# Kernel optimization log

Measured on AMD Instinct MI355X. Metric: run time of the kernel, lower is better.

Reference implementation:

```python
import jax, jax.numpy as jnp
import numpy as np

B, S, H = 4, 1024, 4096
NH, NKV, HD = 32, 8, 128
LEVEL = 256


def lsq_quant(x, s, sym):
    # LSQ fake quantization with grad-scale on s and STE round.
    if sym:
        qn, qp = -LEVEL // 2, LEVEL // 2 - 1
    else:
        qn, qp = 0, LEVEL - 1
    g = 1.0 / np.sqrt(x.size * qp)
    s_sc = s * g + jax.lax.stop_gradient(s - s * g)  # value == s, grad scaled by g
    xs = jnp.clip(x / s_sc, qn, qp)
    xq = xs + jax.lax.stop_gradient(jnp.round(xs) - xs)  # STE round
    return xq * s_sc


def rotate_half(x):
    d = x.shape[-1] // 2
    return jnp.concatenate([-x[..., d:], x[..., :d]], axis=-1)


def setup_inputs() -> dict:
    key = jax.random.key(0)
    ks = jax.random.split(key, 8)
    hidden_states = jax.random.normal(ks[0], (B, S, H), dtype=jnp.float32)
    # real RoPE tables (theta=10000)
    inv_freq = 1.0 / (10000.0 ** (np.arange(0, HD, 2, dtype=np.float32) / HD))
    pos = np.arange(S, dtype=np.float32)
    freqs = np.outer(pos, inv_freq)                      # [S, HD/2]
    emb = np.concatenate([freqs, freqs], axis=-1)        # [S, HD]
    cos = jnp.broadcast_to(jnp.cos(emb)[None], (B, S, HD)).astype(jnp.float32)
    sin = jnp.broadcast_to(jnp.sin(emb)[None], (B, S, HD)).astype(jnp.float32)
    # additive causal mask [B,1,S,S]
    neg = jnp.finfo(jnp.float32).min
    causal = jnp.where(jnp.tril(jnp.ones((S, S), bool)), 0.0, neg)
    attention_mask = jnp.broadcast_to(causal[None, None], (B, 1, S, S)).astype(jnp.float32)
    std = 1.0 / np.sqrt(H)
    Wq = jax.random.normal(ks[1], (NH * HD, H), dtype=jnp.float32) * std
    Wk = jax.random.normal(ks[2], (NKV * HD, H), dtype=jnp.float32) * std
    Wv = jax.random.normal(ks[3], (NKV * HD, H), dtype=jnp.float32) * std
    Wo = jax.random.normal(ks[4], (H, NH * HD), dtype=jnp.float32) * std
    return {
        "hidden_states": hidden_states, "cos": cos, "sin": sin,
        "attention_mask": attention_mask,
        "Wq": Wq, "Wk": Wk, "Wv": Wv, "Wo": Wo,
        "s_q": jnp.float32(0.05), "s_k": jnp.float32(0.05), "s_v": jnp.float32(0.05),
        "s_attn": jnp.float32(0.05), "s_after": jnp.float32(0.05), "s_o": jnp.float32(0.05),
    }


def reference(hidden_states, cos, sin, attention_mask, Wq, Wk, Wv, Wo,
              s_q, s_k, s_v, s_attn, s_after, s_o):
    b, s, _ = hidden_states.shape
    scaling = HD ** -0.5
    n_rep = NH // NKV
    # projections (torch Linear: x @ W^T), reshape to [B, heads, S, HD]
    q = (hidden_states @ Wq.T).reshape(b, s, NH, HD).transpose(0, 2, 1, 3)
    k = (hidden_states @ Wk.T).reshape(b, s, NKV, HD).transpose(0, 2, 1, 3)
    v = (hidden_states @ Wv.T).reshape(b, s, NKV, HD).transpose(0, 2, 1, 3)
    q = lsq_quant(q, s_q, sym=True)
    k = lsq_quant(k, s_k, sym=True)
    v = lsq_quant(v, s_v, sym=True)
    # rotary embeddings (cos/sin: [B,S,HD] -> broadcast over head dim)
    c = cos[:, None, :, :]
    sn = sin[:, None, :, :]
    q = q * c + rotate_half(q) * sn
    k = k * c + rotate_half(k) * sn
    # repeat KV heads for GQA
    k = jnp.repeat(k, n_rep, axis=1)
    v = jnp.repeat(v, n_rep, axis=1)
    attn = jnp.einsum('bhqd,bhkd->bhqk', q, k) * scaling
    attn = lsq_quant(attn, s_attn, sym=False)
    attn = attn + attention_mask
    attn = jax.nn.softmax(attn.astype(jnp.float32), axis=-1)
    out = jnp.einsum('bhqk,bhkd->bhqd', attn, v)
    out = lsq_quant(out, s_after, sym=False)
    out = out.transpose(0, 2, 1, 3).reshape(b, s, NH * HD)
    out = out @ Wo.T
    out = lsq_quant(out, s_o, sym=True)
    return out, attn
```

## Files before the change

kernel.cpp:

```cpp
#include <hip/hip_runtime.h>
#include <math.h>

#define B_   4
#define S_   1024
#define H_   4096
#define NH_  32
#define NKV_ 8
#define HD_  128
#define M_   (B_*S_)
#define LDF16 12288
#define SCALING 0.08838834764831845f


typedef _Float16 f16;
typedef __attribute__((ext_vector_type(4))) _Float16 f16x4;
typedef __attribute__((ext_vector_type(8))) _Float16 f16x8;
typedef __attribute__((ext_vector_type(4))) float f32x4;

__device__ __forceinline__ float lsq_sym(float x, float s) {
  float xs = x / s;
  xs = fminf(fmaxf(xs, -128.0f), 127.0f);
  return rintf(xs) * s;
}
__device__ __forceinline__ float lsq_asym(float x, float s) {
  float xs = x / s;
  xs = fminf(fmaxf(xs, 0.0f), 255.0f);
  return rintf(xs) * s;
}

struct f16pair { f16 hi, lo; };
__device__ __forceinline__ f16pair cvt_hilo(float x) {
  f16pair r;
  r.hi = (f16)x;
  r.lo = (f16)(x - (float)r.hi);
  return r;
}

__device__ __forceinline__ void gload16(const void* g, void* l) {
  __builtin_amdgcn_global_load_lds((const __attribute__((address_space(1))) void*)g,
                                   (__attribute__((address_space(3))) void*)l, 16, 0, 0);
}

__global__ __launch_bounds__(256)
void split_flat(const float* __restrict__ src, f16* __restrict__ hi, f16* __restrict__ lo)
{
  const size_t i = ((size_t)blockIdx.x * 256 + threadIdx.x) * 4;
  float4 v = *(const float4*)(src + i);
  f16x4 h, l; f16pair p;
  p = cvt_hilo(v.x); h.x = p.hi; l.x = p.lo;
  p = cvt_hilo(v.y); h.y = p.hi; l.y = p.lo;
  p = cvt_hilo(v.z); h.z = p.hi; l.z = p.lo;
  p = cvt_hilo(v.w); h.w = p.hi; l.w = p.lo;
  *(f16x4*)(hi + i) = h;
  *(f16x4*)(lo + i) = l;
}

__global__ __launch_bounds__(256)
void split_wqk(const float* __restrict__ W, f16* __restrict__ hi, f16* __restrict__ lo, int ldw)
{
  const size_t i = ((size_t)blockIdx.x * 256 + threadIdx.x) * 4;
  const int n = (int)(i / ldw);
  const int k = (int)(i % ldw);
  const int d = n & 127;
  const int prow = (n & ~127) | ((d < 64) ? (d << 1) : (((d - 64) << 1) | 1));
  float4 v = *(const float4*)(W + i);
  f16x4 h, l; f16pair p;
  p = cvt_hilo(v.x); h.x = p.hi; l.x = p.lo;
  p = cvt_hilo(v.y); h.y = p.hi; l.y = p.lo;
  p = cvt_hilo(v.z); h.z = p.hi; l.z = p.lo;
  p = cvt_hilo(v.w); h.w = p.hi; l.w = p.lo;
  *(f16x4*)(hi + (size_t)prow * ldw + k) = h;
  *(f16x4*)(lo + (size_t)prow * ldw + k) = l;
}

__global__ __launch_bounds__(256)
void split_wo(const float* __restrict__ Wo, f16* __restrict__ base)
{
  const size_t i = ((size_t)blockIdx.x * 256 + threadIdx.x) * 4;
  const int n = (int)(i >> 12);
  const int k = (int)(i & 4095);
  float4 v = *(const float4*)(Wo + i);
  f16x4 h, l; f16pair p;
  p = cvt_hilo(v.x); h.x = p.hi; l.x = p.lo;
  p = cvt_hilo(v.y); h.y = p.hi; l.y = p.lo;
  p = cvt_hilo(v.z); h.z = p.hi; l.z = p.lo;
  p = cvt_hilo(v.w); h.w = p.hi; l.w = p.lo;
  f16* rp = base + (size_t)n * LDF16;
  *(f16x4*)(rp + 4096 + k) = h;
  *(f16x4*)(rp + 8192 + k) = l;
}

template<int ATERMS, int EPI>
__global__ __launch_bounds__(256, 2)
void gemm_mfma(const f16* __restrict__ Ahi, const f16* __restrict__ Alo, int lda,
               const f16* __restrict__ Bhi, const f16* __restrict__ Blo, int ldb,
               float* __restrict__ C, int ldc, int K,
               const float* __restrict__ sA, const float* __restrict__ sQ,
               const float* __restrict__ cosp, const float* __restrict__ sinp,
               f16* __restrict__ oBase, int hiOff, int loOff)
{
  __shared__ f16 sAh[256 * 32];
  __shared__ f16 sAl[(ATERMS == 2) ? 256 * 32 : 64];
  __shared__ f16 sBh[128 * 32];
  __shared__ f16 sBl[128 * 32];

  const int m0 = blockIdx.y << 8;
  const int n0 = blockIdx.x << 7;
  const int t    = threadIdx.x;
  const int lane = t & 63;
  const int wv   = t >> 6;
  const int wm   = (wv >> 1) << 7;
  const int wn   = (wv & 1) << 6;
  const int lrow = lane & 15;
  const int kg   = (lane >> 4) << 3;
  const int fsw  = (lrow & 3) << 3;

  const int sr   = lane >> 2;
  const int slot = lane & 3;
  const int kcs  = ((slot ^ (sr & 3)) << 3);

  f32x4 acc[8][4];
  #pragma unroll
  for (int i = 0; i < 8; ++i)
    #pragma unroll
    for (int j = 0; j < 4; ++j) acc[i][j] = (f32x4){0.f, 0.f, 0.f, 0.f};

  for (int k0 = 0; k0 < K; k0 += 32) {
    #pragma unroll
    for (int i = 0; i < 4; ++i) {
      const int rowb = (wv << 6) + (i << 4);
      const size_t goff = (size_t)(m0 + rowb + sr) * lda + k0 + kcs;
      gload16(Ahi + goff, &sAh[rowb * 32]);
      if constexpr (ATERMS == 2) gload16(Alo + goff, &sAl[rowb * 32]);
    }
    #pragma unroll
    for (int i = 0; i < 2; ++i) {
      const int rowb = (wv << 5) + (i << 4);
      const size_t goff = (size_t)(n0 + rowb + sr) * ldb + k0 + kcs;
      gload16(Bhi + goff, &sBh[rowb * 32]);
      gload16(Blo + goff, &sBl[rowb * 32]);
    }
    __syncthreads();

    f16x8 a[8], bh[4], bl[4];
    #pragma unroll
    for (int j = 0; j < 4; ++j) {
      const int r = wn + (j << 4) + lrow;
      bh[j] = *(const f16x8*)&sBh[r * 32 + (kg ^ fsw)];
      bl[j] = *(const f16x8*)&sBl[r * 32 + (kg ^ fsw)];
    }
    #pragma unroll
    for (int i = 0; i < 8; ++i)
      a[i] = *(const f16x8*)&sAh[(wm + (i << 4) + lrow) * 32 + (kg ^ fsw)];
    #pragma unroll
    for (int i = 0; i < 8; ++i)
      #pragma unroll
      for (int j = 0; j < 4; ++j) {
        acc[i][j] = __builtin_amdgcn_mfma_f32_16x16x32_f16(a[i], bh[j], acc[i][j], 0, 0, 0);
        acc[i][j] = __builtin_amdgcn_mfma_f32_16x16x32_f16(a[i], bl[j], acc[i][j], 0, 0, 0);
      }
    if constexpr (ATERMS == 2) {
      #pragma unroll
      for (int i = 0; i < 8; ++i)
        a[i] = *(const f16x8*)&sAl[(wm + (i << 4) + lrow) * 32 + (kg ^ fsw)];
      #pragma unroll
      for (int i = 0; i < 8; ++i)
        #pragma unroll
        for (int j = 0; j < 4; ++j)
          acc[i][j] = __builtin_amdgcn_mfma_f32_16x16x32_f16(a[i], bh[j], acc[i][j], 0, 0, 0);
    }
    __syncthreads();
  }

  const float s = *sA;
  float sQv = 1.0f;
  if constexpr (EPI == 1) sQv = *sQ;

  #pragma unroll
  for (int i = 0; i < 8; ++i)
    #pragma unroll
    for (int j = 0; j < 4; ++j) {
      const int gc = n0 + wn + (j << 4) + lrow;
      #pragma unroll
      for (int r = 0; r < 4; ++r) {
        const int gr = m0 + wm + (i << 4) + ((lane >> 4) << 2) + r;
        float x = acc[i][j][r];
        if constexpr (EPI == 1) {
          C[(size_t)gr * ldc + gc] = lsq_sym(x * s, sQv);
        } else if constexpr (EPI == 2) {
          float qv = lsq_sym(x, s);
          float pv = __shfl_xor(qv, 1);
          const int dpair = (gc & 127) >> 1;
          float cs = cosp[(size_t)gr * HD_ + dpair];
          float sn = sinp[(size_t)gr * HD_ + dpair];
          float ro = (gc & 1) ? (qv * cs + pv * sn) : (qv * cs - pv * sn);
          f16pair hp = cvt_hilo(ro);
          f16* o = oBase + (size_t)gr * LDF16;
          o[hiOff + gc] = hp.hi;
          o[loOff + gc] = hp.lo;
        } else {
          float xi = rintf(fminf(fmaxf(x / s, -128.0f), 127.0f));
          const int bb = gr >> 10, ss = gr & 1023;
          const int kv = gc >> 7,  dd = gc & 127;
          const size_t f = ((size_t)((bb * 8 + kv) * 128 + dd) << 10) + ss;
          oBase[(f >> 10) * LDF16 + 11264 + (f & 1023)] = (f16)xi;
        }
      }
    }
}

__global__ __launch_bounds__(256)
void attn_fused(const f16* __restrict__ fqkv, float* __restrict__ attn,
                const float* __restrict__ saP)
{
  const int b = blockIdx.z, h = blockIdx.y, qi0 = blockIdx.x << 4;
  const int t = threadIdx.x, lane = t & 63, w = t >> 6;
  const int lc = lane & 15, lg = lane >> 4;
  const int kvh = h >> 2;
  const float sa = *saP;

  f16x8 qh[4], ql[4];
  {
    const f16* qrow = fqkv + (size_t)(b * S_ + qi0 + lc) * LDF16 + h * HD_;
    #pragma unroll
    for (int c = 0; c < 4; ++c) {
      const int off = c * 32 + lg * 8;
      qh[c] = *(const f16x8*)(qrow + off);
      ql[c] = *(const f16x8*)(qrow + 4096 + off);
    }
  }

  f32x4 acc[16];
  #pragma unroll
  for (int tt = 0; tt < 16; ++tt) acc[tt] = (f32x4){0.f, 0.f, 0.f, 0.f};

  const int qimax = qi0 + 15;
  const f16* kbase = fqkv + (size_t)(b * S_) * LDF16 + 8192 + kvh * HD_;

  #pragma unroll
  for (int tt = 0; tt < 16; ++tt) {
    const int ki0 = (w << 8) + (tt << 4);
    if (ki0 <= qimax) {
      const f16* krow = kbase + (size_t)(ki0 + lc) * LDF16;
      #pragma unroll
      for (int c = 0; c < 4; ++c) {
        const int off = c * 32 + lg * 8;
        f16x8 kh = *(const f16x8*)(krow + off);
        f16x8 kl = *(const f16x8*)(krow + 1024 + off);
        acc[tt] = __builtin_amdgcn_mfma_f32_16x16x32_f16(qh[c], kh, acc[tt], 0, 0, 0);
        acc[tt] = __builtin_amdgcn_mfma_f32_16x16x32_f16(ql[c], kh, acc[tt], 0, 0, 0);
        acc[tt] = __builtin_amdgcn_mfma_f32_16x16x32_f16(qh[c], kl, acc[tt], 0, 0, 0);
      }
    }
  }

  float m4[4] = {-3.0e38f, -3.0e38f, -3.0e38f, -3.0e38f};
  #pragma unroll
  for (int tt = 0; tt < 16; ++tt) {
    const int ki = (w << 8) + (tt << 4) + lc;
    #pragma unroll
    for (int r = 0; r < 4; ++r) {
      const int qi = qi0 + lg * 4 + r;
      float x = (ki <= qi) ? lsq_asym(acc[tt][r] * SCALING, sa) : -3.0e38f;
      acc[tt][r] = x;
      m4[r] = fmaxf(m4[r], x);
    }
  }
  #pragma unroll
  for (int off = 1; off < 16; off <<= 1)
    #pragma unroll
    for (int r = 0; r < 4; ++r) m4[r] = fmaxf(m4[r], __shfl_xor(m4[r], off));

  __shared__ float red[4][16];
  if (lc == 0) {
    #pragma unroll
    for (int r = 0; r < 4; ++r) red[w][lg * 4 + r] = m4[r];
  }
  __syncthreads();
  float mrow[4];
  #pragma unroll
  for (int r = 0; r < 4; ++r) {
    const int row = lg * 4 + r;
    mrow[r] = fmaxf(fmaxf(red[0][row], red[1][row]), fmaxf(red[2][row], red[3][row]));
  }
  __syncthreads();

  float s4[4] = {0.f, 0.f, 0.f, 0.f};
  #pragma unroll
  for (int tt = 0; tt < 16; ++tt)
    #pragma unroll
    for (int r = 0; r < 4; ++r) {
      float p = expf(acc[tt][r] - mrow[r]);
      acc[tt][r] = p;
      s4[r] += p;
    }
  #pragma unroll
  for (int off = 1; off < 16; off <<= 1)
    #pragma unroll
    for (int r = 0; r < 4; ++r) s4[r] += __shfl_xor(s4[r], off);
  if (lc == 0) {
    #pragma unroll
    for (int r = 0; r < 4; ++r) red[w][lg * 4 + r] = s4[r];
  }
  __syncthreads();
  float inv[4];
  #pragma unroll
  for (int r = 0; r < 4; ++r) {
    const int row = lg * 4 + r;
    inv[r] = 1.0f / (red[0][row] + red[1][row] + red[2][row] + red[3][row]);
  }

  #pragma unroll
  for (int tt = 0; tt < 16; ++tt) {
    const int ki = (w << 8) + (tt << 4) + lc;
    #pragma unroll
    for (int r = 0; r < 4; ++r) {
      const int qi = qi0 + lg * 4 + r;
      attn[((size_t)(b * NH_ + h) * S_ + qi) * S_ + ki] = acc[tt][r] * inv[r];
    }
  }
}

__global__ __launch_bounds__(256)
void pv_mfma(const float* __restrict__ attn, f16* __restrict__ fqkv,
             const float* __restrict__ svP, const float* __restrict__ safP)
{
  const int b = blockIdx.z, h = blockIdx.y, q0 = blockIdx.x << 7;
  const int t = threadIdx.x, lane = t & 63, w = t >> 6;
  const int wd = (w >> 1) << 6, wq = (w & 1) << 6;
  const int lc = lane & 15, lg = lane >> 4;
  const int kvh = h >> 2;
  const float sv = *svP, saf = *safP;

  f32x4 acc[4][4];
  #pragma unroll
  for (int i = 0; i < 4; ++i)
    #pragma unroll
    for (int j = 0; j < 4; ++j) acc[i][j] = (f32x4){0.f, 0.f, 0.f, 0.f};

  const float* Pbase = attn + (size_t)(b * NH_ + h) * S_ * S_;
  const int kimax = q0 + 128;

  for (int ki0 = 0; ki0 < kimax; ki0 += 32) {
    f16x8 a[4];
    #pragma unroll
    for (int i = 0; i < 4; ++i) {
      const int d = wd + i * 16 + lc;
      const size_t f = ((size_t)((b * 8 + kvh) * 128 + d) << 10) + ki0 + lg * 8;
      a[i] = *(const f16x8*)(fqkv + (f >> 10) * LDF16 + 11264 + (f & 1023));
    }
    #pragma unroll
    for (int j = 0; j < 4; ++j) {
      const int q = q0 + wq + j * 16 + lc;
      const float* pp = Pbase + (size_t)q * S_ + ki0 + lg * 8;
      float4 p0 = *(const float4*)pp;
      float4 p1 = *(const float4*)(pp + 4);
      f16x8 bh, bl; f16pair pr;
      pr = cvt_hilo(p0.x); bh[0] = pr.hi; bl[0] = pr.lo;
      pr = cvt_hilo(p0.y); bh[1] = pr.hi; bl[1] = pr.lo;
      pr = cvt_hilo(p0.z); bh[2] = pr.hi; bl[2] = pr.lo;
      pr = cvt_hilo(p0.w); bh[3] = pr.hi; bl[3] = pr.lo;
      pr = cvt_hilo(p1.x); bh[4] = pr.hi; bl[4] = pr.lo;
      pr = cvt_hilo(p1.y); bh[5] = pr.hi; bl[5] = pr.lo;
      pr = cvt_hilo(p1.z); bh[6] = pr.hi; bl[6] = pr.lo;
      pr = cvt_hilo(p1.w); bh[7] = pr.hi; bl[7] = pr.lo;
      #pragma unroll
      for (int i = 0; i < 4; ++i) {
        acc[i][j] = __builtin_amdgcn_mfma_f32_16x16x32_f16(a[i], bh, acc[i][j], 0, 0, 0);
        acc[i][j] = __builtin_amdgcn_mfma_f32_16x16x32_f16(a[i], bl, acc[i][j], 0, 0, 0);
      }
    }
  }

  #pragma unroll
  for (int i = 0; i < 4; ++i)
    #pragma unroll
    for (int j = 0; j < 4; ++j) {
      const int q  = q0 + wq + j * 16 + lc;
      const int d0 = wd + i * 16 + lg * 4;
      f16x4 v;
      #pragma unroll
      for (int r = 0; r < 4; ++r) {
        float x = sv * acc[i][j][r];
        x = fminf(fmaxf(x / saf, 0.0f), 255.0f);
        v[r] = (f16)rintf(x);
      }
      *(f16x4*)(fqkv + (size_t)(b * S_ + q) * LDF16 + h * HD_ + d0) = v;
    }
}

extern "C" void kernel_launch(void* const* d_in, const int* in_sizes, int n_in,
                              void* d_out, int out_size, void* d_ws, size_t ws_size,
                              hipStream_t stream)
{
  const float* hidden = (const float*)d_in[0];
  const float* cosp   = (const float*)d_in[1];
  const float* sinp   = (const float*)d_in[2];
  const float* Wq     = (const float*)d_in[4];
  const float* Wk     = (const float*)d_in[5];
  const float* Wv     = (const float*)d_in[6];
  const float* Wo     = (const float*)d_in[7];
  const float* s_q    = (const float*)d_in[8];
  const float* s_k    = (const float*)d_in[9];
  const float* s_v    = (const float*)d_in[10];
  const float* s_attn = (const float*)d_in[11];
  const float* s_after= (const float*)d_in[12];
  const float* s_o    = (const float*)d_in[13];

  float* out  = (float*)d_out;
  float* attn = out + (size_t)M_ * H_;
  f16*  f16qkv = (f16*)d_ws;

  f16* scr = (f16*)attn;
  f16* hHi = scr;
  f16* hLo = scr + (size_t)16777216;
  f16* wHi = scr + (size_t)2 * 16777216;
  f16* wLo = scr + (size_t)3 * 16777216;

  dim3 blk(256, 1, 1);

  split_flat<<<dim3(16384), blk, 0, stream>>>(hidden, hHi, hLo);
  split_wqk<<<dim3(16384), blk, 0, stream>>>(Wq, wHi, wLo, H_);
  gemm_mfma<2,2><<<dim3(32,16), blk, 0, stream>>>(hHi, hLo, H_, wHi, wLo, H_,
      nullptr, 0, H_, s_q, nullptr, cosp, sinp, f16qkv, 0, 4096);
  split_wqk<<<dim3(4096), blk, 0, stream>>>(Wk, wHi, wLo, H_);
  gemm_mfma<2,2><<<dim3(8,16), blk, 0, stream>>>(hHi, hLo, H_, wHi, wLo, H_,
      nullptr, 0, H_, s_k, nullptr, cosp, sinp, f16qkv, 8192, 9216);

  split_flat<<<dim3(4096), blk, 0, stream>>>(Wv, wHi, wLo);
  gemm_mfma<2,3><<<dim3(8,16), blk, 0, stream>>>(hHi, hLo, H_, wHi, wLo, H_,
      nullptr, 0, H_, s_v, nullptr, nullptr, nullptr, f16qkv, 0, 0);

  attn_fused<<<dim3(64, NH_, B_), blk, 0, stream>>>(f16qkv, attn, s_attn);

  pv_mfma<<<dim3(8, NH_, B_), blk, 0, stream>>>(attn, f16qkv, s_v, s_after);

  split_wo<<<dim3(16384), blk, 0, stream>>>(Wo, f16qkv);
  gemm_mfma<1,1><<<dim3(32,16), blk, 0, stream>>>(f16qkv, nullptr, LDF16,
      f16qkv + 4096, f16qkv + 8192, LDF16,
      out, H_, H_, s_after, s_o, nullptr, nullptr, nullptr, 0, 0);
}
```

Measured before the change: 1.841 ms.

## Transpose QK MFMA operands for row-contiguous float4 attn stores, use 8 waves

The attention score kernel swaps the MFMA A/B operands so each lane holds four consecutive key columns of one query row. That allows float4 stores to the attn matrix instead of scattered scalar stores. The block grows to 512 threads (8 waves of 128 keys each), which halves per-thread accumulators, and softmax now uses the fast __expf. It also hardcodes the weight split stride to shifts. The costs are more waves for the LDS reduction and slightly lower exp accuracy.

```diff
diff --git a/kernel.cpp b/kernel.cpp
--- a/kernel.cpp
+++ b/kernel.cpp
@@ -56,11 +56,11 @@
 }
 
 __global__ __launch_bounds__(256)
-void split_wqk(const float* __restrict__ W, f16* __restrict__ hi, f16* __restrict__ lo, int ldw)
+void split_wqk(const float* __restrict__ W, f16* __restrict__ hi, f16* __restrict__ lo)
 {
   const size_t i = ((size_t)blockIdx.x * 256 + threadIdx.x) * 4;
-  const int n = (int)(i / ldw);
-  const int k = (int)(i % ldw);
+  const int n = (int)(i >> 12);
+  const int k = (int)(i & 4095);
   const int d = n & 127;
   const int prow = (n & ~127) | ((d < 64) ? (d << 1) : (((d - 64) << 1) | 1));
   float4 v = *(const float4*)(W + i);
@@ -69,8 +69,8 @@
   p = cvt_hilo(v.y); h.y = p.hi; l.y = p.lo;
   p = cvt_hilo(v.z); h.z = p.hi; l.z = p.lo;
   p = cvt_hilo(v.w); h.w = p.hi; l.w = p.lo;
-  *(f16x4*)(hi + (size_t)prow * ldw + k) = h;
-  *(f16x4*)(lo + (size_t)prow * ldw + k) = l;
+  *(f16x4*)(hi + (size_t)prow * 4096 + k) = h;
+  *(f16x4*)(lo + (size_t)prow * 4096 + k) = l;
 }
 
 __global__ __launch_bounds__(256)
@@ -209,7 +209,7 @@
     }
 }
 
-__global__ __launch_bounds__(256)
+__global__ __launch_bounds__(512)
 void attn_fused(const f16* __restrict__ fqkv, float* __restrict__ attn,
                 const float* __restrict__ saP)
 {
@@ -230,16 +230,16 @@
     }
   }
 
-  f32x4 acc[16];
-  #pragma unroll
-  for (int tt = 0; tt < 16; ++tt) acc[tt] = (f32x4){0.f, 0.f, 0.f, 0.f};
+  f32x4 acc[8];
+  #pragma unroll
+  for (int tt = 0; tt < 8; ++tt) acc[tt] = (f32x4){0.f, 0.f, 0.f, 0.f};
 
   const int qimax = qi0 + 15;
   const f16* kbase = fqkv + (size_t)(b * S_) * LDF16 + 8192 + kvh * HD_;
 
   #pragma unroll
-  for (int tt = 0; tt < 16; ++tt) {
-    const int ki0 = (w << 8) + (tt << 4);
+  for (int tt = 0; tt < 8; ++tt) {
+    const int ki0 = (w << 7) + (tt << 4);
     if (ki0 <= qimax) {
       const f16* krow = kbase + (size_t)(ki0 + lc) * LDF16;
       #pragma unroll
@@ -247,77 +247,65 @@
         const int off = c * 32 + lg * 8;
         f16x8 kh = *(const f16x8*)(krow + off);
         f16x8 kl = *(const f16x8*)(krow + 1024 + off);
-        acc[tt] = __builtin_amdgcn_mfma_f32_16x16x32_f16(qh[c], kh, acc[tt], 0, 0, 0);
-        acc[tt] = __builtin_amdgcn_mfma_f32_16x16x32_f16(ql[c], kh, acc[tt], 0, 0, 0);
-        acc[tt] = __builtin_amdgcn_mfma_f32_16x16x32_f16(qh[c], kl, acc[tt], 0, 0, 0);
+        acc[tt] = __builtin_amdgcn_mfma_f32_16x16x32_f16(kh, qh[c], acc[tt], 0, 0, 0);
+        acc[tt] = __builtin_amdgcn_mfma_f32_16x16x32_f16(kh, ql[c], acc[tt], 0, 0, 0);
+        acc[tt] = __builtin_amdgcn_mfma_f32_16x16x32_f16(kl, qh[c], acc[tt], 0, 0, 0);
       }
     }
   }
 
-  float m4[4] = {-3.0e38f, -3.0e38f, -3.0e38f, -3.0e38f};
-  #pragma unroll
-  for (int tt = 0; tt < 16; ++tt) {
-    const int ki = (w << 8) + (tt << 4) + lc;
+  const int qi = qi0 + lc;
+
+  float m = -3.0e38f;
+  #pragma unroll
+  for (int tt = 0; tt < 8; ++tt) {
+    const int kib = (w << 7) + (tt << 4) + (lg << 2);
     #pragma unroll
     for (int r = 0; r < 4; ++r) {
-      const int qi = qi0 + lg * 4 + r;
-      float x = (ki <= qi) ? lsq_asym(acc[tt][r] * SCALING, sa) : -3.0e38f;
+      float x = (kib + r <= qi) ? lsq_asym(acc[tt][r] * SCALING, sa) : -3.0e38f;
       acc[tt][r] = x;
-      m4[r] = fmaxf(m4[r], x);
-    }
-  }
-  #pragma unroll
-  for (int off = 1; off < 16; off <<= 1)
-    #pragma unroll
-    for (int r = 0; r < 4; ++r) m4[r] = fmaxf(m4[r], __shfl_xor(m4[r], off));
-
-  __shared__ float red[4][16];
-  if (lc == 0) {
-    #pragma unroll
-    for (int r = 0; r < 4; ++r) red[w][lg * 4 + r] = m4[r];
-  }
+      m = fmaxf(m, x);
+    }
+  }
+  m = fmaxf(m, __shfl_xor(m, 16));
+  m = fmaxf(m, __shfl_xor(m, 32));
+
+  __shared__ float redM[8][16];
+  __shared__ float redS[8][16];
+  if (lg == 0) redM[w][lc] = m;
   __syncthreads();
-  float mrow[4];
-  #pragma unroll
-  for (int r = 0; r < 4; ++r) {
-    const int row = lg * 4 + r;
-    mrow[r] = fmaxf(fmaxf(red[0][row], red[1][row]), fmaxf(red[2][row], red[3][row]));
-  }
+  float mrow = redM[0][lc];
+  #pragma unroll
+  for (int ww = 1; ww < 8; ++ww) mrow = fmaxf(mrow, redM[ww][lc]);
+
+  float ssum = 0.f;
+  #pragma unroll
+  for (int tt = 0; tt < 8; ++tt) {
+    #pragma unroll
+    for (int r = 0; r < 4; ++r) {
+      float p = __expf(acc[tt][r] - mrow);
+      acc[tt][r] = p;
+      ssum += p;
+    }
+  }
+  ssum += __shfl_xor(ssum, 16);
+  ssum += __shfl_xor(ssum, 32);
+  if (lg == 0) redS[w][lc] = ssum;
   __syncthreads();
-
-  float s4[4] = {0.f, 0.f, 0.f, 0.f};
-  #pragma unroll
-  for (int tt = 0; tt < 16; ++tt)
-    #pragma unroll
-    for (int r = 0; r < 4; ++r) {
-      float p = expf(acc[tt][r] - mrow[r]);
-      acc[tt][r] = p;
-      s4[r] += p;
-    }
-  #pragma unroll
-  for (int off = 1; off < 16; off <<= 1)
-    #pragma unroll
-    for (int r = 0; r < 4; ++r) s4[r] += __shfl_xor(s4[r], off);
-  if (lc == 0) {
-    #pragma unroll
-    for (int r = 0; r < 4; ++r) red[w][lg * 4 + r] = s4[r];
-  }
-  __syncthreads();
-  float inv[4];
-  #pragma unroll
-  for (int r = 0; r < 4; ++r) {
-    const int row = lg * 4 + r;
-    inv[r] = 1.0f / (red[0][row] + red[1][row] + red[2][row] + red[3][row]);
-  }
-
-  #pragma unroll
-  for (int tt = 0; tt < 16; ++tt) {
-    const int ki = (w << 8) + (tt << 4) + lc;
-    #pragma unroll
-    for (int r = 0; r < 4; ++r) {
-      const int qi = qi0 + lg * 4 + r;
-      attn[((size_t)(b * NH_ + h) * S_ + qi) * S_ + ki] = acc[tt][r] * inv[r];
-    }
+  float tot = redS[0][lc];
+  #pragma unroll
+  for (int ww = 1; ww < 8; ++ww) tot += redS[ww][lc];
+  const float inv = 1.0f / tot;
+
+  float* orow = attn + ((size_t)(b * NH_ + h) * S_ + qi) * S_ + (w << 7) + (lg << 2);
+  #pragma unroll
+  for (int tt = 0; tt < 8; ++tt) {
+    float4 v;
+    v.x = acc[tt][0] * inv;
+    v.y = acc[tt][1] * inv;
+    v.z = acc[tt][2] * inv;
+    v.w = acc[tt][3] * inv;
+    *(float4*)(orow + (tt << 4)) = v;
   }
 }
 
@@ -420,10 +408,10 @@
   dim3 blk(256, 1, 1);
 
   split_flat<<<dim3(16384), blk, 0, stream>>>(hidden, hHi, hLo);
-  split_wqk<<<dim3(16384), blk, 0, stream>>>(Wq, wHi, wLo, H_);
+  split_wqk<<<dim3(16384), blk, 0, stream>>>(Wq, wHi, wLo);
   gemm_mfma<2,2><<<dim3(32,16), blk, 0, stream>>>(hHi, hLo, H_, wHi, wLo, H_,
       nullptr, 0, H_, s_q, nullptr, cosp, sinp, f16qkv, 0, 4096);
-  split_wqk<<<dim3(4096), blk, 0, stream>>>(Wk, wHi, wLo, H_);
+  split_wqk<<<dim3(4096), blk, 0, stream>>>(Wk, wHi, wLo);
   gemm_mfma<2,2><<<dim3(8,16), blk, 0, stream>>>(hHi, hLo, H_, wHi, wLo, H_,
       nullptr, 0, H_, s_k, nullptr, cosp, sinp, f16qkv, 8192, 9216);
 
@@ -431,7 +419,7 @@
   gemm_mfma<2,3><<<dim3(8,16), blk, 0, stream>>>(hHi, hLo, H_, wHi, wLo, H_,
       nullptr, 0, H_, s_v, nullptr, nullptr, nullptr, f16qkv, 0, 0);
 
-  attn_fused<<<dim3(64, NH_, B_), blk, 0, stream>>>(f16qkv, attn, s_attn);
+  attn_fused<<<dim3(64, NH_, B_), dim3(512,1,1), 0, stream>>>(f16qkv, attn, s_attn);
 
   pv_mfma<<<dim3(8, NH_, B_), blk, 0, stream>>>(attn, f16qkv, s_v, s_after);
 
```

Result: slower. 1.887 ms (+2.5%).
